# Kernel tuning notes

Hardware: AMD Instinct MI355X
Metric: run time of the kernel (lower is better)

## Reference

```python
import jax, jax.numpy as jnp
import numpy as np

B, T, C = 4, 2048, 1024
H = 16
HS = C // H  # 64
FF = 4 * C  # 4096


def setup_inputs() -> dict:
    key = jax.random.key(0)
    ks = jax.random.split(key, 10)
    s_in = C ** -0.5
    s_ff = FF ** -0.5
    return {
        "x": jax.random.normal(ks[0], (B, T, C), dtype=jnp.float32),
        "Wq": jax.random.normal(ks[1], (H, C, HS), dtype=jnp.float32) * s_in,
        "Wk": jax.random.normal(ks[2], (H, C, HS), dtype=jnp.float32) * s_in,
        "Wv": jax.random.normal(ks[3], (H, C, HS), dtype=jnp.float32) * s_in,
        "Wproj": jax.random.normal(ks[4], (C, C), dtype=jnp.float32) * s_in,
        "bproj": jax.random.normal(ks[5], (C,), dtype=jnp.float32) * 0.01,
        "W1": jax.random.normal(ks[6], (C, FF), dtype=jnp.float32) * s_in,
        "b1": jax.random.normal(ks[7], (FF,), dtype=jnp.float32) * 0.01,
        "W2": jax.random.normal(ks[8], (FF, C), dtype=jnp.float32) * s_ff,
        "b2": jax.random.normal(ks[9], (C,), dtype=jnp.float32) * 0.01,
    }


def reference(x, Wq, Wk, Wv, Wproj, bproj, W1, b1, W2, b2):
    b, t, c = x.shape
    # per-head projections, batched over heads: [B,H,T,HS]
    q = jnp.einsum("btc,hcd->bhtd", x, Wq)
    k = jnp.einsum("btc,hcd->bhtd", x, Wk)
    v = jnp.einsum("btc,hcd->bhtd", x, Wv)
    # NOTE: original scales by full embed dim c**-0.5, not head_size
    scores = jnp.einsum("bhtd,bhsd->bhts", q, k) * (c ** -0.5)
    causal = jnp.tril(jnp.ones((t, t), dtype=bool))
    scores = jnp.where(causal[None, None], scores, -jnp.inf)
    w = jax.nn.softmax(scores, axis=-1)
    y = jnp.einsum("bhts,bhsd->bhtd", w, v)  # [B,H,T,HS]
    y = jnp.transpose(y, (0, 2, 1, 3)).reshape(b, t, c)  # concat heads
    attn_out = y @ Wproj + bproj
    x = attn_out + x
    ff = jax.nn.relu(x @ W1 + b1) @ W2 + b2
    return ff + x
```

## Files before the change

### kernel.cpp

```cpp
#include <hip/hip_runtime.h>

typedef unsigned short u16;
typedef __attribute__((ext_vector_type(4))) float f32x4;
typedef __attribute__((ext_vector_type(8))) short bf16x8;

constexpr int kB  = 4;
constexpr int kT  = 2048;
constexpr int kC  = 1024;
constexpr int kH  = 16;
constexpr int kFF = 4096;
constexpr int kM  = kB * kT;
constexpr int k3C = 3 * kC;

__device__ __forceinline__ float b2f(u16 u) {
    union { unsigned int i; float f; } v;
    v.i = ((unsigned int)u) << 16;
    return v.f;
}
__device__ __forceinline__ u16 f2b(float f) {
    union { float f; unsigned int i; } v;
    v.f = f;
    unsigned int r = (v.i + 0x7FFFu + ((v.i >> 16) & 1u)) >> 16;
    return (u16)r;
}

__device__ __forceinline__ void lds_barrier() {
    __asm__ __volatile__("" ::: "memory");
    __builtin_amdgcn_s_waitcnt(0xC07F);
    __builtin_amdgcn_s_barrier();
    __asm__ __volatile__("" ::: "memory");
}

__global__ void cvt_f32_bf16(const float* __restrict__ in, u16* __restrict__ out, int n4)
{
    const int i = blockIdx.x * 256 + threadIdx.x;
    if (i >= n4) return;
    float4 v = *(const float4*)(in + (size_t)i * 4);
    ushort4 o;
    o.x = f2b(v.x); o.y = f2b(v.y); o.z = f2b(v.z); o.w = f2b(v.w);
    *(ushort4*)(out + (size_t)i * 4) = o;
}

__global__ void transpose_cvt(const float* __restrict__ in, int R, int Cc,
                              u16* __restrict__ out)
{
    __shared__ float t[32][33];
    const int bx = blockIdx.x * 32;
    const int by = blockIdx.y * 32;
    const int lx = threadIdx.x, ly = threadIdx.y;
    #pragma unroll
    for (int i = 0; i < 32; i += 8)
        t[ly + i][lx] = in[(size_t)(by + ly + i) * Cc + bx + lx];
    __syncthreads();
    #pragma unroll
    for (int i = 0; i < 32; i += 8)
        out[(size_t)(bx + ly + i) * R + by + lx] = f2b(t[lx][ly + i]);
}

__global__ void repack_qkv_t(const float* __restrict__ Wq, const float* __restrict__ Wk,
                             const float* __restrict__ Wv, u16* __restrict__ out)
{
    __shared__ float t[32][33];
    const int z = blockIdx.z;
    const int s = z >> 4, h = z & 15;
    const float* in = (s == 0 ? Wq : s == 1 ? Wk : Wv) + (size_t)h * (kC * 64);
    const int bx = blockIdx.x * 32;
    const int by = blockIdx.y * 32;
    const int lx = threadIdx.x, ly = threadIdx.y;
    #pragma unroll
    for (int i = 0; i < 32; i += 8)
        t[ly + i][lx] = in[(size_t)(by + ly + i) * 64 + bx + lx];
    __syncthreads();
    const int orow = s * kC + h * 64 + bx;
    #pragma unroll
    for (int i = 0; i < 32; i += 8)
        out[(size_t)(orow + ly + i) * kC + by + lx] = f2b(t[lx][ly + i]);
}

__global__ __launch_bounds__(512, 4) void gemm_bt_k32r(
    const u16* __restrict__ A, int lda,
    const u16* __restrict__ Bt, int ldb,
    int K,
    const float* __restrict__ bias,
    const u16* __restrict__ resid,
    float* __restrict__ CoF,
    u16* __restrict__ CoB,
    int ldc, int do_relu, int nbx)
{
    __shared__ __align__(16) u16 As[3][256 * 32];
    __shared__ __align__(16) u16 Bs[3][128 * 32];

    const int tid  = threadIdx.x;
    const int wave = tid >> 6, lane = tid & 63;
    const int wm = (wave >> 1) * 64, wn = (wave & 1) * 64;

    const int cpx = gridDim.x >> 3;
    const int swz = (blockIdx.x & 7) * cpx + (blockIdx.x >> 3);
    const int bx = swz % nbx, by = swz / nbx;
    const int m0 = by * 256, n0 = bx * 128;

    const int rl = tid >> 2;
    const int cg = ((tid & 3) ^ ((tid >> 3) & 3)) * 8;

    const int fm = lane & 15, fkq = lane >> 4;
    const int fchunk = (fkq ^ ((fm >> 1) & 3)) * 8;

    f32x4 acc[4][4];
    #pragma unroll
    for (int i = 0; i < 4; ++i)
        #pragma unroll
        for (int j = 0; j < 4; ++j)
            acc[i][j] = (f32x4){0.f, 0.f, 0.f, 0.f};

    const int NT = K >> 5;

    auto stg = [&](const u16* g, int ld, int r0, u16* l) {
        __builtin_amdgcn_global_load_lds(
            (const __attribute__((address_space(1))) void*)(g + (size_t)(r0 + rl) * ld + cg),
            (__attribute__((address_space(3))) void*)(l + r0 * 32 + tid * 8), 16, 0, 0);
    };
    auto stageAB = [&](int kt, int slot) {
        const u16* ga = A  + (size_t)m0 * lda + kt * 32;
        const u16* gb = Bt + (size_t)n0 * ldb + kt * 32;
        stg(ga, lda, 0,   As[slot]);
        stg(ga, lda, 128, As[slot]);
        stg(gb, ldb, 0,   Bs[slot]);
    };

    stageAB(0, 0);
    if (NT > 1) {
        stageAB(1, 1);
        __builtin_amdgcn_sched_barrier(0);
        __asm__ __volatile__("s_waitcnt vmcnt(3)" ::: "memory");
    } else {
        __builtin_amdgcn_sched_barrier(0);
        __asm__ __volatile__("s_waitcnt vmcnt(0)" ::: "memory");
    }
    __builtin_amdgcn_s_barrier();
    __builtin_amdgcn_sched_barrier(0);

    int cur = 0;
    for (int t = 0; t < NT; ++t) {
        const int sst = (cur == 0) ? 2 : cur - 1;
        if (t + 2 < NT) stageAB(t + 2, sst);
        const u16* Sa = As[cur];
        const u16* Sb = Bs[cur];
        bf16x8 a[4], b[4];
        #pragma unroll
        for (int i = 0; i < 4; ++i) {
            const int m = wm + i * 16 + fm;
            a[i] = *(const bf16x8*)&Sa[m * 32 + fchunk];
        }
        #pragma unroll
        for (int j = 0; j < 4; ++j) {
            const int n = wn + j * 16 + fm;
            b[j] = *(const bf16x8*)&Sb[n * 32 + fchunk];
        }
        __builtin_amdgcn_s_setprio(1);
        #pragma unroll
        for (int i = 0; i < 4; ++i)
            #pragma unroll
            for (int j = 0; j < 4; ++j)
                acc[i][j] = __builtin_amdgcn_mfma_f32_16x16x32_bf16(
                    a[i], b[j], acc[i][j], 0, 0, 0);
        __builtin_amdgcn_s_setprio(0);
        if (t + 1 < NT) {
            __builtin_amdgcn_sched_barrier(0);
            if (t + 2 < NT) { __asm__ __volatile__("s_waitcnt vmcnt(3)" ::: "memory"); }
            else            { __asm__ __volatile__("s_waitcnt vmcnt(0)" ::: "memory"); }
            __builtin_amdgcn_s_barrier();
            __builtin_amdgcn_sched_barrier(0);
        }
        cur = (cur == 2) ? 0 : cur + 1;
    }

    const int col = lane & 15;
    const int rb  = (lane >> 4) * 4;
    #pragma unroll
    for (int i = 0; i < 4; ++i) {
        #pragma unroll
        for (int j = 0; j < 4; ++j) {
            const int n = n0 + wn + j * 16 + col;
            #pragma unroll
            for (int r = 0; r < 4; ++r) {
                const int m = m0 + wm + i * 16 + rb + r;
                float v = acc[i][j][r];
                if (bias)    v += bias[n];
                if (do_relu) v = fmaxf(v, 0.f);
                if (resid)   v += b2f(resid[(size_t)m * ldc + n]);
                if (CoF) CoF[(size_t)m * ldc + n] = v;
                else     CoB[(size_t)m * ldc + n] = f2b(v);
            }
        }
    }
}

__global__ __launch_bounds__(256) void attn_mfma3(
    const u16* __restrict__ QKV, u16* __restrict__ Y)
{
    __shared__ __align__(16) u16 Kl[2][64 * 64];
    __shared__ __align__(16) u16 Vt[2][64 * 64];
    __shared__ __align__(16) u16 Pl[4][16 * 64];

    const int tid  = threadIdx.x;
    const int wave = tid >> 6, lane = tid & 63;
    const int ln = lane & 15, quad = lane >> 4;
    const int idx = blockIdx.x;
    const int bh = idx & 63;
    const int qt = 15 - (idx >> 6);
    const int b = bh >> 4, h = bh & 15;
    const int q0 = qt << 7;
    const int bT = b * kT;
    const int qgw = q0 + wave * 32;
    const float scale = 0.03125f;

    const u16* kvbase = QKV + (size_t)bT * k3C + kC + h * 64;

    const int sK = tid >> 3, cK = tid & 7;
    const int sV = (tid >> 3) * 2, cV = tid & 7;
    const int kwa0 = (sK << 6) + ((cK ^ (sK & 7)) << 3);
    const int kwa1 = kwa0 + (32 << 6);

    bf16x8 qa[2][2];
    #pragma unroll
    for (int qsub = 0; qsub < 2; ++qsub) {
        const size_t qb = ((size_t)bT + qgw + 16 * qsub + ln) * k3C + h * 64;
        qa[qsub][0] = *(const bf16x8*)(QKV + qb + quad * 8);
        qa[qsub][1] = *(const bf16x8*)(QKV + qb + 32 + quad * 8);
    }

    f32x4 acco[2][4];
    #pragma unroll
    for (int qsub = 0; qsub < 2; ++qsub)
        #pragma unroll
        for (int jd = 0; jd < 4; ++jd) acco[qsub][jd] = (f32x4){0.f, 0.f, 0.f, 0.f};
    float mrun[2] = {-1e30f, -1e30f}, lrun[2] = {0.f, 0.f};
    u16* Pw = Pl[wave];

    const int ntiles = 2 * qt + 2;

    auto loadkv = [&](int s0p, uint4& k0, uint4& k1, uint4& v0, uint4& v1) {
        const u16* kg = kvbase + (size_t)(s0p + sK) * k3C + cK * 8;
        k0 = *(const uint4*)kg;
        k1 = *(const uint4*)(kg + (size_t)32 * k3C);
        const u16* vg = kvbase + kC + (size_t)(s0p + sV) * k3C + cV * 8;
        v0 = *(const uint4*)vg;
        v1 = *(const uint4*)(vg + k3C);
    };
    auto stage = [&](u16* Kb, u16* Vb, const uint4& k0, const uint4& k1,
                     const uint4& v0, const uint4& v1) {
        *(uint4*)&Kb[kwa0] = k0;
        *(uint4*)&Kb[kwa1] = k1;
        const u16* t0 = (const u16*)&v0;
        const u16* t1 = (const u16*)&v1;
        #pragma unroll
        for (int i = 0; i < 8; ++i) {
            const int d = cV * 8 + i;
            const int chunk = ((sV >> 3) ^ (d & 7) ^ ((d >> 3) & 7)) & 7;
            ushort2 pr; pr.x = t0[i]; pr.y = t1[i];
            *(ushort2*)&Vb[(d << 6) + (chunk << 3) + (sV & 7)] = pr;
        }
    };
    auto compute = [&](int t, const u16* Kb, const u16* Vb) {
        const int s0 = t << 6;
        if (s0 > qgw + 31) return;
        f32x4 accs[2][4];
        #pragma unroll
        for (int qsub = 0; qsub < 2; ++qsub)
            #pragma unroll
            for (int j = 0; j < 4; ++j) accs[qsub][j] = (f32x4){0.f, 0.f, 0.f, 0.f};
        #pragma unroll
        for (int ks = 0; ks < 2; ++ks) {
            #pragma unroll
            for (int j = 0; j < 4; ++j) {
                const int s = j * 16 + ln;
                bf16x8 kb = *(const bf16x8*)&Kb[(s << 6) + ((((quad + 4 * ks) ^ (s & 7)) & 7) << 3)];
                accs[0][j] = __builtin_amdgcn_mfma_f32_16x16x32_bf16(kb, qa[0][ks], accs[0][j], 0, 0, 0);
                accs[1][j] = __builtin_amdgcn_mfma_f32_16x16x32_bf16(kb, qa[1][ks], accs[1][j], 0, 0, 0);
            }
        }
        bf16x8 vfr[4][2];
        #pragma unroll
        for (int jd = 0; jd < 4; ++jd) {
            const int d = jd * 16 + ln;
            #pragma unroll
            for (int ks = 0; ks < 2; ++ks)
                vfr[jd][ks] = *(const bf16x8*)&Vb[(d << 6) + ((((quad + 4 * ks) ^ (d & 7) ^ ((d >> 3) & 7)) & 7) << 3)];
        }
        #pragma unroll
        for (int qsub = 0; qsub < 2; ++qsub) {
            const int qg = qgw + 16 * qsub + ln;
            float part = -1e30f;
            #pragma unroll
            for (int j = 0; j < 4; ++j) {
                #pragma unroll
                for (int r = 0; r < 4; ++r) {
                    const int sg = s0 + j * 16 + quad * 4 + r;
                    float v = accs[qsub][j][r] * scale;
                    v = (sg <= qg) ? v : -1e30f;
                    accs[qsub][j][r] = v;
                    part = fmaxf(part, v);
                }
            }
            float mx = fmaxf(part, __shfl_xor(part, 16));
            mx = fmaxf(mx, __shfl_xor(mx, 32));
            const float mn = fmaxf(mrun[qsub], mx);
            const float al = __expf(mrun[qsub] - mn);
            mrun[qsub] = mn;
            float ls = 0.f;
            #pragma unroll
            for (int j = 0; j < 4; ++j)
                #pragma unroll
                for (int r = 0; r < 4; ++r) {
                    const float p = __expf(accs[qsub][j][r] - mn);
                    accs[qsub][j][r] = p;
                    ls += p;
                }
            ls += __shfl_xor(ls, 16);
            ls += __shfl_xor(ls, 32);
            lrun[qsub] = lrun[qsub] * al + ls;
            #pragma unroll
            for (int jd = 0; jd < 4; ++jd)
                #pragma unroll
                for (int r = 0; r < 4; ++r)
                    acco[qsub][jd][r] *= al;
            #pragma unroll
            for (int j = 0; j < 4; ++j) {
                ushort4 pk;
                pk.x = f2b(accs[qsub][j][0]); pk.y = f2b(accs[qsub][j][1]);
                pk.z = f2b(accs[qsub][j][2]); pk.w = f2b(accs[qsub][j][3]);
                const int chunk = ((2 * j + (quad >> 1)) ^ (ln & 7)) & 7;
                *(ushort4*)&Pw[(ln << 6) + (chunk << 3) + ((quad & 1) << 2)] = pk;
            }
            #pragma unroll
            for (int ks = 0; ks < 2; ++ks) {
                bf16x8 pb = *(const bf16x8*)&Pw[(ln << 6) + ((((4 * ks + quad) ^ (ln & 7)) & 7) << 3)];
                #pragma unroll
                for (int jd = 0; jd < 4; ++jd)
                    acco[qsub][jd] = __builtin_amdgcn_mfma_f32_16x16x32_bf16(
                        vfr[jd][ks], pb, acco[qsub][jd], 0, 0, 0);
            }
        }
    };

    uint4 ka0, ka1, va0, va1, kb0, kb1, vb0, vb1;
    loadkv(0, ka0, ka1, va0, va1);
    for (int t = 0; t < ntiles; t += 2) {
        stage(Kl[0], Vt[0], ka0, ka1, va0, va1);
        loadkv((t + 1) << 6, kb0, kb1, vb0, vb1);
        lds_barrier();
        compute(t, Kl[0], Vt[0]);
        stage(Kl[1], Vt[1], kb0, kb1, vb0, vb1);
        loadkv(((t + 2) < ntiles ? (t + 2) : 0) << 6, ka0, ka1, va0, va1);
        lds_barrier();
        compute(t + 1, Kl[1], Vt[1]);
    }

    #pragma unroll
    for (int qsub = 0; qsub < 2; ++qsub) {
        const float inv = 1.f / lrun[qsub];
        const size_t yrow = ((size_t)bT + qgw + 16 * qsub + ln) * kC + h * 64;
        #pragma unroll
        for (int jd = 0; jd < 4; ++jd) {
            ushort4 ov;
            ov.x = f2b(acco[qsub][jd][0] * inv);
            ov.y = f2b(acco[qsub][jd][1] * inv);
            ov.z = f2b(acco[qsub][jd][2] * inv);
            ov.w = f2b(acco[qsub][jd][3] * inv);
            *(ushort4*)(Y + yrow + jd * 16 + quad * 4) = ov;
        }
    }
}

extern "C" void kernel_launch(void* const* d_in, const int* in_sizes, int n_in,
                              void* d_out, int out_size, void* d_ws, size_t ws_size,
                              hipStream_t stream) {
    const float* x     = (const float*)d_in[0];
    const float* Wq    = (const float*)d_in[1];
    const float* Wk    = (const float*)d_in[2];
    const float* Wv    = (const float*)d_in[3];
    const float* Wproj = (const float*)d_in[4];
    const float* bproj = (const float*)d_in[5];
    const float* W1    = (const float*)d_in[6];
    const float* b1    = (const float*)d_in[7];
    const float* W2    = (const float*)d_in[8];
    const float* b2    = (const float*)d_in[9];

    u16* ws      = (u16*)d_ws;
    u16* QKV     = ws;
    u16* ffh     = ws;
    u16* attn_y  = ws + (size_t)kM * kFF;
    u16* xb      = attn_y  + (size_t)kM * kC;
    u16* res1    = xb      + (size_t)kM * kC;
    u16* Wqkv_t  = res1    + (size_t)kM * kC;
    u16* Wproj_t = Wqkv_t  + (size_t)k3C * kC;
    u16* W1t     = Wproj_t + (size_t)kC * kC;
    u16* W2t     = W1t     + (size_t)kFF * kC;
    float* out   = (float*)d_out;

    cvt_f32_bf16<<<(kM * kC / 4 + 255) / 256, 256, 0, stream>>>(x, xb, kM * kC / 4);
    repack_qkv_t<<<dim3(2, kC / 32, 48), dim3(32, 8), 0, stream>>>(Wq, Wk, Wv, Wqkv_t);
    transpose_cvt<<<dim3(kC / 32, kC / 32),  dim3(32, 8), 0, stream>>>(Wproj, kC, kC, Wproj_t);
    transpose_cvt<<<dim3(kFF / 32, kC / 32), dim3(32, 8), 0, stream>>>(W1, kC, kFF, W1t);
    transpose_cvt<<<dim3(kC / 32, kFF / 32), dim3(32, 8), 0, stream>>>(W2, kFF, kC, W2t);

    gemm_bt_k32r<<<dim3((kM / 256) * (k3C / 128)), 512, 0, stream>>>(
        xb, kC, Wqkv_t, kC, kC, nullptr, nullptr, nullptr, QKV, k3C, 0, k3C / 128);
    attn_mfma3<<<dim3(1024), 256, 0, stream>>>(QKV, attn_y);
    gemm_bt_k32r<<<dim3((kM / 256) * (kC / 128)), 512, 0, stream>>>(
        attn_y, kC, Wproj_t, kC, kC, bproj, xb, nullptr, res1, kC, 0, kC / 128);
    gemm_bt_k32r<<<dim3((kM / 256) * (kFF / 128)), 512, 0, stream>>>(
        res1, kC, W1t, kC, kC, b1, nullptr, nullptr, ffh, kFF, 1, kFF / 128);
    gemm_bt_k32r<<<dim3((kM / 256) * (kC / 128)), 512, 0, stream>>>(
        ffh, kFF, W2t, kFF, kFF, b2, res1, out, nullptr, kC, 0, kC / 128);
}
```

Baseline: 567.3 us.

## Use 256x256 tile GEMM for FFN and split-K the down-projection

Adds a new GEMM kernel with 256x256 output tiles (each wave computes 128x64), double-buffered LDS staging through global_load_lds, and an optional two-way split-K. The kernel is used for both FFN GEMMs. The W2 GEMM is split along K into two halves, the second half writes an fp32 partial buffer, and an extra elementwise kernel adds the partial into the output. The larger tiles raise arithmetic intensity and cut operand reloads. Split-K keeps the grid large enough for the down-projection. The cost is higher register and LDS pressure, fewer blocks for W1, and an extra fp32 read/write pass over the output.

New measurement: 1.748 ms. 3.08x slower.

```diff
diff --git a/kernel.cpp b/kernel.cpp
--- a/kernel.cpp
+++ b/kernel.cpp
@@ -31,6 +31,13 @@
     __asm__ __volatile__("" ::: "memory");
 }
 
+__device__ __forceinline__ void tile_barrier() {
+    __builtin_amdgcn_sched_barrier(0);
+    __asm__ __volatile__("s_waitcnt vmcnt(0)" ::: "memory");
+    __builtin_amdgcn_s_barrier();
+    __builtin_amdgcn_sched_barrier(0);
+}
+
 __global__ void cvt_f32_bf16(const float* __restrict__ in, u16* __restrict__ out, int n4)
 {
     const int i = blockIdx.x * 256 + threadIdx.x;
@@ -39,6 +46,16 @@
     ushort4 o;
     o.x = f2b(v.x); o.y = f2b(v.y); o.z = f2b(v.z); o.w = f2b(v.w);
     *(ushort4*)(out + (size_t)i * 4) = o;
+}
+
+__global__ void add_f32(float* __restrict__ out, const float* __restrict__ part, int n4)
+{
+    const int i = blockIdx.x * 256 + threadIdx.x;
+    if (i >= n4) return;
+    float4 a = *(const float4*)(out + (size_t)i * 4);
+    float4 b = *(const float4*)(part + (size_t)i * 4);
+    a.x += b.x; a.y += b.y; a.z += b.z; a.w += b.w;
+    *(float4*)(out + (size_t)i * 4) = a;
 }
 
 __global__ void transpose_cvt(const float* __restrict__ in, int R, int Cc,
@@ -75,6 +92,117 @@
     #pragma unroll
     for (int i = 0; i < 32; i += 8)
         out[(size_t)(orow + ly + i) * kC + by + lx] = f2b(t[lx][ly + i]);
+}
+
+__global__ __launch_bounds__(512, 4) void gemm_bt_256sq(
+    const u16* __restrict__ A, int lda,
+    const u16* __restrict__ Bt, int ldb,
+    int K,
+    const float* __restrict__ bias,
+    const u16* __restrict__ resid,
+    float* __restrict__ CoF,
+    u16* __restrict__ CoB,
+    int ldc, int do_relu, int nbx,
+    int ksplit, float* __restrict__ Cpart)
+{
+    __shared__ __align__(16) u16 As[2][256 * 32];
+    __shared__ __align__(16) u16 Bs[2][256 * 32];
+
+    const int tid  = threadIdx.x;
+    const int wave = tid >> 6, lane = tid & 63;
+    const int wm = (wave >> 2) * 128, wn = (wave & 3) * 64;
+
+    int bidx = blockIdx.x, nb = gridDim.x, kh = 0;
+    if (ksplit) { kh = bidx & 1; bidx >>= 1; nb >>= 1; }
+    const int cpx = nb >> 3;
+    const int swz = (bidx & 7) * cpx + (bidx >> 3);
+    const int bx = swz % nbx, by = swz / nbx;
+    const int m0 = by * 256, n0 = bx * 256;
+    const int koff = kh * K;
+
+    const int rl = tid >> 2;
+    const int cg = ((tid & 3) ^ ((tid >> 3) & 3)) * 8;
+
+    const int fm = lane & 15, fkq = lane >> 4;
+    const int fchunk = (fkq ^ ((fm >> 1) & 3)) * 8;
+
+    f32x4 acc[8][4];
+    #pragma unroll
+    for (int i = 0; i < 8; ++i)
+        #pragma unroll
+        for (int j = 0; j < 4; ++j)
+            acc[i][j] = (f32x4){0.f, 0.f, 0.f, 0.f};
+
+    const int NT = K >> 5;
+
+    auto stg = [&](const u16* g, int ld, int r0, u16* l) {
+        __builtin_amdgcn_global_load_lds(
+            (const __attribute__((address_space(1))) void*)(g + (size_t)(r0 + rl) * ld + cg),
+            (__attribute__((address_space(3))) void*)(l + r0 * 32 + tid * 8), 16, 0, 0);
+    };
+    auto stageAB = [&](int kt) {
+        const u16* ga = A  + (size_t)m0 * lda + koff + kt * 32;
+        const u16* gb = Bt + (size_t)n0 * ldb + koff + kt * 32;
+        stg(ga, lda, 0,   As[kt & 1]);
+        stg(ga, lda, 128, As[kt & 1]);
+        stg(gb, ldb, 0,   Bs[kt & 1]);
+        stg(gb, ldb, 128, Bs[kt & 1]);
+    };
+
+    stageAB(0);
+    tile_barrier();
+
+    for (int t = 0; t < NT; ++t) {
+        if (t + 1 < NT) stageAB(t + 1);
+        const u16* Sa = As[t & 1];
+        const u16* Sb = Bs[t & 1];
+        bf16x8 a[8], b[4];
+        #pragma unroll
+        for (int i = 0; i < 8; ++i) {
+            const int m = wm + i * 16 + fm;
+            a[i] = *(const bf16x8*)&Sa[m * 32 + fchunk];
+        }
+        #pragma unroll
+        for (int j = 0; j < 4; ++j) {
+            const int n = wn + j * 16 + fm;
+            b[j] = *(const bf16x8*)&Sb[n * 32 + fchunk];
+        }
+        __builtin_amdgcn_s_setprio(1);
+        #pragma unroll
+        for (int i = 0; i < 8; ++i)
+            #pragma unroll
+            for (int j = 0; j < 4; ++j)
+                acc[i][j] = __builtin_amdgcn_mfma_f32_16x16x32_bf16(
+                    a[i], b[j], acc[i][j], 0, 0, 0);
+        __builtin_amdgcn_s_setprio(0);
+        if (t + 1 < NT) tile_barrier();
+    }
+
+    const float* bp = bias;
+    const u16*   rp = resid;
+    float* cf = CoF;
+    u16*   cb = CoB;
+    if (ksplit && kh) { bp = nullptr; rp = nullptr; cf = Cpart; cb = nullptr; }
+
+    const int col = lane & 15;
+    const int rb  = (lane >> 4) * 4;
+    #pragma unroll
+    for (int i = 0; i < 8; ++i) {
+        #pragma unroll
+        for (int j = 0; j < 4; ++j) {
+            const int n = n0 + wn + j * 16 + col;
+            #pragma unroll
+            for (int r = 0; r < 4; ++r) {
+                const int m = m0 + wm + i * 16 + rb + r;
+                float v = acc[i][j][r];
+                if (bp)      v += bp[n];
+                if (do_relu) v = fmaxf(v, 0.f);
+                if (rp)      v += b2f(rp[(size_t)m * ldc + n]);
+                if (cf) cf[(size_t)m * ldc + n] = v;
+                else    cb[(size_t)m * ldc + n] = f2b(v);
+            }
+        }
+    }
 }
 
 __global__ __launch_bounds__(512, 4) void gemm_bt_k32r(
@@ -396,6 +524,7 @@
     u16* Wproj_t = Wqkv_t  + (size_t)k3C * kC;
     u16* W1t     = Wproj_t + (size_t)kC * kC;
     u16* W2t     = W1t     + (size_t)kFF * kC;
+    float* Cpart = (float*)(ws + (size_t)kM * kFF);
     float* out   = (float*)d_out;
 
     cvt_f32_bf16<<<(kM * kC / 4 + 255) / 256, 256, 0, stream>>>(x, xb, kM * kC / 4);
@@ -409,8 +538,11 @@
     attn_mfma3<<<dim3(1024), 256, 0, stream>>>(QKV, attn_y);
     gemm_bt_k32r<<<dim3((kM / 256) * (kC / 128)), 512, 0, stream>>>(
         attn_y, kC, Wproj_t, kC, kC, bproj, xb, nullptr, res1, kC, 0, kC / 128);
-    gemm_bt_k32r<<<dim3((kM / 256) * (kFF / 128)), 512, 0, stream>>>(
-        res1, kC, W1t, kC, kC, b1, nullptr, nullptr, ffh, kFF, 1, kFF / 128);
-    gemm_bt_k32r<<<dim3((kM / 256) * (kC / 128)), 512, 0, stream>>>(
-        ffh, kFF, W2t, kFF, kFF, b2, res1, out, nullptr, kC, 0, kC / 128);
-}
+    gemm_bt_256sq<<<dim3((kM / 256) * (kFF / 256)), 512, 0, stream>>>(
+        res1, kC, W1t, kC, kC, b1, nullptr, nullptr, ffh, kFF, 1, kFF / 256,
+        0, nullptr);
+    gemm_bt_256sq<<<dim3(2 * (kM / 256) * (kC / 256)), 512, 0, stream>>>(
+        ffh, kFF, W2t, kFF, kFF / 2, b2, res1, out, nullptr, kC, 0, kC / 256,
+        1, Cpart);
+    add_f32<<<dim3(kM * kC / 4 / 256), 256, 0, stream>>>(out, Cpart, kM * kC / 4);
+}
```
